# Optimization experiments

Measured on AMD Instinct MI355X. Metric: run time of the kernel, lower is better.

Reference implementation:

```python
import jax, jax.numpy as jnp
import numpy as np

B, N, K, H = 4, 2048, 30, 8
NUM_HIDDEN, NUM_IN, NUM_LATENT = 512, 640, 128
D = NUM_HIDDEN // H


def setup_inputs() -> dict:
    key = jax.random.key(0)
    ks = jax.random.split(key, 10)
    s = 0.05
    return {
        "z": jax.random.normal(ks[0], (B, NUM_LATENT), jnp.float32),
        "h_V": jax.random.normal(ks[1], (B, N, NUM_HIDDEN), jnp.float32),
        "h_E": jax.random.normal(ks[2], (B, N, K, NUM_IN), jnp.float32),
        "mask_attend": jnp.ones((B, N, K), jnp.float32),
        # weights stored as (in, out); torch Linear computes x @ W.T
        "W_Q": jax.random.normal(ks[3], (NUM_HIDDEN, NUM_HIDDEN), jnp.float32) * s,
        "W_K": jax.random.normal(ks[4], (NUM_IN, NUM_HIDDEN), jnp.float32) * s,
        "W_V": jax.random.normal(ks[5], (NUM_IN, NUM_HIDDEN), jnp.float32) * s,
        "W_O": jax.random.normal(ks[6], (NUM_HIDDEN, NUM_HIDDEN), jnp.float32) * s,
        "W_z": jax.random.normal(ks[7], (NUM_LATENT, K * H), jnp.float32) * s,
        "W_b": jax.random.normal(ks[8], (NUM_IN - 33, H), jnp.float32) * s,
    }


def reference(z, h_V, h_E, mask_attend, W_Q, W_K, W_V, W_O, W_z, W_b):
    b, n, k, _ = h_E.shape
    # projections
    Q = (h_V @ W_Q).reshape(b, n, H, D)            # [B,N,H,D]
    Kp = (h_E @ W_K).reshape(b, n, k, H, D)        # [B,N,K,H,D]
    V = (h_E @ W_V).reshape(b, n, k, H, D)         # [B,N,K,H,D]
    # per-neighbor dot-product scores -> [B,N,H,K]
    logits = jnp.einsum("bnhd,bnkhd->bnhk", Q, Kp) / np.sqrt(D).astype(np.float32)
    # latent bias: W_z output reshaped as (K, H) then transposed -> [B,1,H,K]
    bias_latent = (z @ W_z).reshape(b, 1, k, H).transpose(0, 1, 3, 2)
    # edge bias from h_E features past index 33 -> [B,N,H,K]
    bias_edges = (h_E[..., 33:] @ W_b).reshape(b, n, k, H).transpose(0, 1, 3, 2)
    logits = logits + bias_latent + bias_edges
    # masked, numerically stable softmax over K neighbors
    mask = mask_attend[:, :, None, :]              # [B,N,1,K] broadcast over heads
    neg_inf = jnp.finfo(jnp.float32).min
    logits = jnp.where(mask > 0, logits, neg_inf)
    attend = jax.nn.softmax(logits, axis=-1) * mask  # [B,N,H,K]
    # weighted aggregation of V, merge heads, output projection
    h_upd = jnp.einsum("bnhk,bnkhd->bnhd", attend, V).reshape(b, n, NUM_HIDDEN)
    return h_upd @ W_O
```

## Files before the change

kernel.cpp:

```cpp
#include <hip/hip_runtime.h>

#define B_      4
#define N_      2048
#define KN      30
#define H_      8
#define D_      64
#define CH      512
#define CI      640
#define CL      128
#define BN_TOT  8192

typedef unsigned short u16;
typedef unsigned int   u32;

typedef __attribute__((ext_vector_type(8))) short bf16x8;
typedef __attribute__((ext_vector_type(4))) float f32x4;

__device__ __forceinline__ float bf2f(u16 u) {
    return __uint_as_float(((u32)u) << 16);
}
__device__ __forceinline__ u16 f2bf(float f) {
    u32 u = __float_as_uint(f);
    return (u16)((u + 0x7FFFu + ((u >> 16) & 1u)) >> 16);
}

#define NEG_INF (-3.4028234663852886e38f)

__device__ __forceinline__ void async16(const void* g, void* l) {
    __builtin_amdgcn_global_load_lds(
        (const __attribute__((address_space(1))) unsigned int*)g,
        (__attribute__((address_space(3))) unsigned int*)l, 16, 0, 0);
}

__global__ __launch_bounds__(256) void cvt_kernel(
    const float* __restrict__ in, u16* __restrict__ out, int n)
{
    int i4 = (blockIdx.x * 256 + threadIdx.x) * 4;
    if (i4 < n) {
        float4 v = *(const float4*)&in[i4];
        ushort4 s;
        s.x = f2bf(v.x); s.y = f2bf(v.y); s.z = f2bf(v.z); s.w = f2bf(v.w);
        *(ushort4*)&out[i4] = s;
    }
}

__global__ __launch_bounds__(256) void cvt_t_kernel(
    const float* __restrict__ in, u16* __restrict__ out, int R, int Cc)
{
    int o = blockIdx.x * 256 + threadIdx.x;
    if (o < R * Cc) {
        int j = o / R, i = o - j * R;
        out[o] = f2bf(in[(size_t)i * Cc + j]);
    }
}

template<int BN, bool BF16OUT>
__global__ __launch_bounds__(256) void mfma_gemm(
    const u16* __restrict__ A, const u16* __restrict__ Bt, void* __restrict__ Cp,
    int K, int lda, int ldb, int ldc,
    long aHead, long bHead, long cHead, float alpha)
{
    constexpr int WN = BN / 2;
    constexpr int NT = WN / 16;
    constexpr int BR = (BN * 4) / 256;

    __shared__ u16 lA[128 * 32];
    __shared__ u16 lB[BN * 32];

    const int t    = threadIdx.x;
    const int w    = t >> 6;
    const int lane = t & 63;
    const int fr   = lane & 15;
    const int fq   = lane >> 4;
    const int wm   = w >> 1, wn = w & 1;
    const int m0   = blockIdx.y * 128;
    const int n0   = blockIdx.x * BN;

    const u16* Ah = A  + (size_t)blockIdx.z * aHead;
    const u16* Bh = Bt + (size_t)blockIdx.z * bHead;

    f32x4 zero = {0.f, 0.f, 0.f, 0.f};
    f32x4 acc[4][NT];
#pragma unroll
    for (int i = 0; i < 4; i++)
#pragma unroll
        for (int j = 0; j < NT; j++) acc[i][j] = zero;

    for (int k0 = 0; k0 < K; k0 += 32) {
#pragma unroll
        for (int r = 0; r < 2; r++) {
            int chunk = r * 256 + t;
            async16(Ah + (size_t)(m0 + (chunk >> 2)) * lda + k0 + ((chunk & 3) << 3),
                    &lA[(r * 256 + w * 64) * 8]);
        }
#pragma unroll
        for (int r = 0; r < BR; r++) {
            int chunk = r * 256 + t;
            async16(Bh + (size_t)(n0 + (chunk >> 2)) * ldb + k0 + ((chunk & 3) << 3),
                    &lB[(r * 256 + w * 64) * 8]);
        }
        __syncthreads();

        bf16x8 af[4], bfr[NT];
#pragma unroll
        for (int i = 0; i < 4; i++)
            af[i] = *(const bf16x8*)&lA[(wm * 64 + i * 16 + fr) * 32 + fq * 8];
#pragma unroll
        for (int j = 0; j < NT; j++)
            bfr[j] = *(const bf16x8*)&lB[(wn * WN + j * 16 + fr) * 32 + fq * 8];
#pragma unroll
        for (int i = 0; i < 4; i++)
#pragma unroll
            for (int j = 0; j < NT; j++)
                acc[i][j] = __builtin_amdgcn_mfma_f32_16x16x32_bf16(
                    af[i], bfr[j], acc[i][j], 0, 0, 0);
        __syncthreads();
    }

    const size_t cbase = (size_t)blockIdx.z * cHead;
#pragma unroll
    for (int i = 0; i < 4; i++) {
        int row = m0 + wm * 64 + i * 16 + fq * 4;
#pragma unroll
        for (int j = 0; j < NT; j++) {
            int col = n0 + wn * WN + j * 16 + fr;
#pragma unroll
            for (int r = 0; r < 4; r++) {
                float v = acc[i][j][r] * alpha;
                if (BF16OUT)
                    ((u16*)Cp)[cbase + (size_t)(row + r) * ldc + col] = f2bf(v);
                else
                    ((float*)Cp)[cbase + (size_t)(row + r) * ldc + col] = v;
            }
        }
    }
}

__global__ __launch_bounds__(256) void biasl_kernel(
    const float* __restrict__ z, const float* __restrict__ Wz,
    float* __restrict__ biasL)
{
    const int t = threadIdx.x;
    if (t < KN * H_) {
        for (int b = 0; b < B_; b++) {
            float s = 0.f;
            for (int l = 0; l < CL; l++) s += z[b * CL + l] * Wz[l * (KN * H_) + t];
            biasL[b * (KN * H_) + t] = s;
        }
    }
}

#define LDE 644

__global__ __launch_bounds__(256) void attn_kernel(
    const float* __restrict__ hE, const float* __restrict__ mask,
    const u16* Qt, const float* __restrict__ Wb,
    const float* __restrict__ biasL, u16* Eagg)
{
    __shared__ u16   ehs[KN * LDE];
    __shared__ float logit_s[H_ * KN];
    __shared__ float att_s[KN * H_];
    __shared__ float mask_s[KN];

    const int bn = blockIdx.x;
    const int b  = bn >> 11;
    const int t  = threadIdx.x;

    const float* he = hE + (size_t)bn * KN * CI;
    for (int idx = t; idx < KN * CI / 4; idx += 256) {
        int k = idx / 160;
        int c = (idx - k * 160) << 2;
        float4 v = *(const float4*)&he[k * CI + c];
        ushort4 sv;
        sv.x = f2bf(v.x); sv.y = f2bf(v.y); sv.z = f2bf(v.z); sv.w = f2bf(v.w);
        *(ushort4*)&ehs[k * LDE + c] = sv;
    }
    if (t < KN) mask_s[t] = mask[(size_t)bn * KN + t];
    __syncthreads();

    if (t < H_ * KN) {
        int h = t / KN, k = t - (t / KN) * KN;
        const u16* qrow = Qt + ((size_t)bn * H_ + h) * CI;
        const u16* erow = &ehs[k * LDE];
        float acc = 0.f;
        for (int c = 0; c < CI; c += 4) {
            ushort4 ev = *(const ushort4*)&erow[c];
            ushort4 qv = *(const ushort4*)&qrow[c];
            acc += bf2f(ev.x) * bf2f(qv.x) + bf2f(ev.y) * bf2f(qv.y)
                 + bf2f(ev.z) * bf2f(qv.z) + bf2f(ev.w) * bf2f(qv.w);
        }
        float acc2 = bf2f(erow[33]) * Wb[0 * H_ + h]
                   + bf2f(erow[34]) * Wb[1 * H_ + h]
                   + bf2f(erow[35]) * Wb[2 * H_ + h];
        for (int c = 36; c < CI; c += 4) {
            ushort4 ev = *(const ushort4*)&erow[c];
            const float* wb = &Wb[(c - 33) * H_ + h];
            acc2 += bf2f(ev.x) * wb[0] + bf2f(ev.y) * wb[8]
                  + bf2f(ev.z) * wb[16] + bf2f(ev.w) * wb[24];
        }
        float lg = acc + acc2 + biasL[b * (KN * H_) + k * H_ + h];
        lg = (mask_s[k] > 0.f) ? lg : NEG_INF;
        logit_s[h * KN + k] = lg;
    }
    __syncthreads();

    if (t < H_) {
        const int h = t;
        float m = NEG_INF;
#pragma unroll
        for (int k = 0; k < KN; k++) m = fmaxf(m, logit_s[h * KN + k]);
        float e[KN];
        float s = 0.f;
#pragma unroll
        for (int k = 0; k < KN; k++) { e[k] = __expf(logit_s[h * KN + k] - m); s += e[k]; }
        float inv = 1.f / s;
#pragma unroll
        for (int k = 0; k < KN; k++) att_s[k * H_ + h] = e[k] * inv * mask_s[k];
    }
    __syncthreads();

    if (t < 160) {
        const int c0 = t << 2;
        float acc[8][4] = {};
        for (int k = 0; k < KN; k++) {
            ushort4 ev = *(const ushort4*)&ehs[k * LDE + c0];
            float f0 = bf2f(ev.x), f1 = bf2f(ev.y), f2 = bf2f(ev.z), f3 = bf2f(ev.w);
            float4 a0 = *(const float4*)&att_s[k * H_];
            float4 a1 = *(const float4*)&att_s[k * H_ + 4];
            float aw[8] = {a0.x, a0.y, a0.z, a0.w, a1.x, a1.y, a1.z, a1.w};
#pragma unroll
            for (int h = 0; h < 8; h++) {
                acc[h][0] += aw[h] * f0; acc[h][1] += aw[h] * f1;
                acc[h][2] += aw[h] * f2; acc[h][3] += aw[h] * f3;
            }
        }
#pragma unroll
        for (int h = 0; h < 8; h++) {
            ushort4 sv;
            sv.x = f2bf(acc[h][0]); sv.y = f2bf(acc[h][1]);
            sv.z = f2bf(acc[h][2]); sv.w = f2bf(acc[h][3]);
            *(ushort4*)&Eagg[((size_t)bn * H_ + h) * CI + c0] = sv;
        }
    }
}

extern "C" void kernel_launch(void* const* d_in, const int* in_sizes, int n_in,
                              void* d_out, int out_size, void* d_ws, size_t ws_size,
                              hipStream_t stream)
{
    const float* z    = (const float*)d_in[0];
    const float* hV   = (const float*)d_in[1];
    const float* hE   = (const float*)d_in[2];
    const float* mask = (const float*)d_in[3];
    const float* WQ   = (const float*)d_in[4];
    const float* WK   = (const float*)d_in[5];
    const float* WV   = (const float*)d_in[6];
    const float* WO   = (const float*)d_in[7];
    const float* Wz   = (const float*)d_in[8];
    const float* Wb   = (const float*)d_in[9];
    float* out = (float*)d_out;

    char* w = (char*)d_ws;
    u16*   hV_bf = (u16*)w;
    u16*   Q_bf  = (u16*)(w + 8388608);
    u16*   Qt    = (u16*)(w + 16777216);
    u16*   WQt   = (u16*)(w + 100663296);
    u16*   WK_bf = (u16*)(w + 101187584);
    u16*   WVt   = (u16*)(w + 101842944);
    u16*   WOt   = (u16*)(w + 102498304);
    float* biasL = (float*)(w + 103022592);
    u16*   Eagg  = Qt;
    u16*   Hupd  = hV_bf;

    cvt_kernel<<<4096, 256, 0, stream>>>(hV, hV_bf, BN_TOT * CH);
    cvt_kernel<<<320, 256, 0, stream>>>(WK, WK_bf, CI * CH);
    cvt_t_kernel<<<1024, 256, 0, stream>>>(WQ, WQt, CH, CH);
    cvt_t_kernel<<<1280, 256, 0, stream>>>(WV, WVt, CI, CH);
    cvt_t_kernel<<<1024, 256, 0, stream>>>(WO, WOt, CH, CH);
    biasl_kernel<<<1, 256, 0, stream>>>(z, Wz, biasL);

    mfma_gemm<128, true><<<dim3(4, 64, 1), 256, 0, stream>>>(
        hV_bf, WQt, Q_bf, CH, CH, CH, CH, 0, 0, 0, 1.0f);
    mfma_gemm<128, true><<<dim3(5, 64, H_), 256, 0, stream>>>(
        Q_bf, WK_bf, Qt, 64, CH, CH, H_ * CI, 64, 64, CI, 0.125f);
    attn_kernel<<<dim3(BN_TOT), 256, 0, stream>>>(hE, mask, Qt, Wb, biasL, Eagg);
    mfma_gemm<64, true><<<dim3(1, 64, H_), 256, 0, stream>>>(
        Eagg, WVt, Hupd, CI, H_ * CI, CI, CH, CI, 64L * CI, 64, 1.0f);
    mfma_gemm<128, false><<<dim3(4, 64, 1), 256, 0, stream>>>(
        Hupd, WOt, out, CH, CH, CH, CH, 0, 0, 0, 1.0f);
}
```

Baseline: 1.291 ms.

## Fold edge bias into Q-tilde GEMM and compute attention logits with MFMA

Adds the W_b edge-bias weights to the per-head projected query vector in the Q·W_K^T GEMM epilogue, so the separate bias dot product over h_E columns disappears from the attention kernel. The logit computation (8 heads × 30 neighbors × 640 channels) now runs as 16x16x32 bf16 MFMAs on two waves instead of scalar FMA loops over 240 threads. The shared-memory h_E tile switches to an XOR-swizzled unpadded layout so the MFMA operand loads avoid bank conflicts. One risk is that the added bias is rounded to bf16 along with Qt, which slightly changes precision. Also, the MFMA rows beyond neighbor 29 are clamped and their duplicate results discarded.

```diff
diff --git a/kernel.cpp b/kernel.cpp
--- a/kernel.cpp
+++ b/kernel.cpp
@@ -54,11 +54,12 @@
     }
 }
 
-template<int BN, bool BF16OUT>
+template<int BN, bool BF16OUT, bool WBIAS>
 __global__ __launch_bounds__(256) void mfma_gemm(
     const u16* __restrict__ A, const u16* __restrict__ Bt, void* __restrict__ Cp,
     int K, int lda, int ldb, int ldc,
-    long aHead, long bHead, long cHead, float alpha)
+    long aHead, long bHead, long cHead, float alpha,
+    const float* __restrict__ wb)
 {
     constexpr int WN = BN / 2;
     constexpr int NT = WN / 16;
@@ -127,6 +128,9 @@
 #pragma unroll
             for (int r = 0; r < 4; r++) {
                 float v = acc[i][j][r] * alpha;
+                if (WBIAS) {
+                    if (col >= 33) v += wb[(size_t)(col - 33) * H_ + blockIdx.z];
+                }
                 if (BF16OUT)
                     ((u16*)Cp)[cbase + (size_t)(row + r) * ldc + col] = f2bf(v);
                 else
@@ -150,21 +154,25 @@
     }
 }
 
-#define LDE 644
+#define LGS 33
 
 __global__ __launch_bounds__(256) void attn_kernel(
     const float* __restrict__ hE, const float* __restrict__ mask,
-    const u16* Qt, const float* __restrict__ Wb,
-    const float* __restrict__ biasL, u16* Eagg)
-{
-    __shared__ u16   ehs[KN * LDE];
-    __shared__ float logit_s[H_ * KN];
+    const u16* Qt, const float* __restrict__ biasL, u16* Eagg)
+{
+    __shared__ __align__(16) u16 ehs[KN * CI];
+    __shared__ float logit_s[H_ * LGS];
     __shared__ float att_s[KN * H_];
     __shared__ float mask_s[KN];
 
-    const int bn = blockIdx.x;
-    const int b  = bn >> 11;
-    const int t  = threadIdx.x;
+    const int bn   = blockIdx.x;
+    const int b    = bn >> 11;
+    const int t    = threadIdx.x;
+    const int w    = t >> 6;
+    const int lane = t & 63;
+    const int fr   = lane & 15;
+    const int fq   = lane >> 4;
+    char* ebase = (char*)ehs;
 
     const float* he = hE + (size_t)bn * KN * CI;
     for (int idx = t; idx < KN * CI / 4; idx += 256) {
@@ -173,34 +181,35 @@
         float4 v = *(const float4*)&he[k * CI + c];
         ushort4 sv;
         sv.x = f2bf(v.x); sv.y = f2bf(v.y); sv.z = f2bf(v.z); sv.w = f2bf(v.w);
-        *(ushort4*)&ehs[k * LDE + c] = sv;
+        *(ushort4*)(ebase + ((k * 1280 + (c << 1)) ^ ((k & 7) << 4))) = sv;
     }
     if (t < KN) mask_s[t] = mask[(size_t)bn * KN + t];
     __syncthreads();
 
-    if (t < H_ * KN) {
-        int h = t / KN, k = t - (t / KN) * KN;
-        const u16* qrow = Qt + ((size_t)bn * H_ + h) * CI;
-        const u16* erow = &ehs[k * LDE];
-        float acc = 0.f;
-        for (int c = 0; c < CI; c += 4) {
-            ushort4 ev = *(const ushort4*)&erow[c];
-            ushort4 qv = *(const ushort4*)&qrow[c];
-            acc += bf2f(ev.x) * bf2f(qv.x) + bf2f(ev.y) * bf2f(qv.y)
-                 + bf2f(ev.z) * bf2f(qv.z) + bf2f(ev.w) * bf2f(qv.w);
-        }
-        float acc2 = bf2f(erow[33]) * Wb[0 * H_ + h]
-                   + bf2f(erow[34]) * Wb[1 * H_ + h]
-                   + bf2f(erow[35]) * Wb[2 * H_ + h];
-        for (int c = 36; c < CI; c += 4) {
-            ushort4 ev = *(const ushort4*)&erow[c];
-            const float* wb = &Wb[(c - 33) * H_ + h];
-            acc2 += bf2f(ev.x) * wb[0] + bf2f(ev.y) * wb[8]
-                  + bf2f(ev.z) * wb[16] + bf2f(ev.w) * wb[24];
-        }
-        float lg = acc + acc2 + biasL[b * (KN * H_) + k * H_ + h];
-        lg = (mask_s[k] > 0.f) ? lg : NEG_INF;
-        logit_s[h * KN + k] = lg;
+    if (w < 2) {
+        const u16* qrow = Qt + (size_t)bn * (H_ * CI) + (fr & 7) * CI + fq * 8;
+        int nr = w * 16 + fr;
+        if (nr > KN - 1) nr = KN - 1;
+        const char* erow = ebase + nr * 1280;
+        const int swz = (nr & 7) << 4;
+        f32x4 lacc = {0.f, 0.f, 0.f, 0.f};
+#pragma unroll 4
+        for (int kk = 0; kk < CI / 32; kk++) {
+            bf16x8 a  = *(const bf16x8*)(qrow + kk * 32);
+            bf16x8 bf = *(const bf16x8*)(erow + ((kk * 64 + fq * 16) ^ swz));
+            lacc = __builtin_amdgcn_mfma_f32_16x16x32_bf16(a, bf, lacc, 0, 0, 0);
+        }
+        int k = w * 16 + fr;
+        if (fq < 2 && k < KN) {
+            float mk = mask_s[k];
+            const float* blp = &biasL[b * (KN * H_) + k * H_];
+#pragma unroll
+            for (int r = 0; r < 4; r++) {
+                int h = fq * 4 + r;
+                float lg = lacc[r] + blp[h];
+                logit_s[h * LGS + k] = (mk > 0.f) ? lg : NEG_INF;
+            }
+        }
     }
     __syncthreads();
 
@@ -208,11 +217,11 @@
         const int h = t;
         float m = NEG_INF;
 #pragma unroll
-        for (int k = 0; k < KN; k++) m = fmaxf(m, logit_s[h * KN + k]);
+        for (int k = 0; k < KN; k++) m = fmaxf(m, logit_s[h * LGS + k]);
         float e[KN];
         float s = 0.f;
 #pragma unroll
-        for (int k = 0; k < KN; k++) { e[k] = __expf(logit_s[h * KN + k] - m); s += e[k]; }
+        for (int k = 0; k < KN; k++) { e[k] = __expf(logit_s[h * LGS + k] - m); s += e[k]; }
         float inv = 1.f / s;
 #pragma unroll
         for (int k = 0; k < KN; k++) att_s[k * H_ + h] = e[k] * inv * mask_s[k];
@@ -223,7 +232,7 @@
         const int c0 = t << 2;
         float acc[8][4] = {};
         for (int k = 0; k < KN; k++) {
-            ushort4 ev = *(const ushort4*)&ehs[k * LDE + c0];
+            ushort4 ev = *(const ushort4*)(ebase + ((k * 1280 + (c0 << 1)) ^ ((k & 7) << 4)));
             float f0 = bf2f(ev.x), f1 = bf2f(ev.y), f2 = bf2f(ev.z), f3 = bf2f(ev.w);
             float4 a0 = *(const float4*)&att_s[k * H_];
             float4 a1 = *(const float4*)&att_s[k * H_ + 4];
@@ -279,13 +288,13 @@
     cvt_t_kernel<<<1024, 256, 0, stream>>>(WO, WOt, CH, CH);
     biasl_kernel<<<1, 256, 0, stream>>>(z, Wz, biasL);
 
-    mfma_gemm<128, true><<<dim3(4, 64, 1), 256, 0, stream>>>(
-        hV_bf, WQt, Q_bf, CH, CH, CH, CH, 0, 0, 0, 1.0f);
-    mfma_gemm<128, true><<<dim3(5, 64, H_), 256, 0, stream>>>(
-        Q_bf, WK_bf, Qt, 64, CH, CH, H_ * CI, 64, 64, CI, 0.125f);
-    attn_kernel<<<dim3(BN_TOT), 256, 0, stream>>>(hE, mask, Qt, Wb, biasL, Eagg);
-    mfma_gemm<64, true><<<dim3(1, 64, H_), 256, 0, stream>>>(
-        Eagg, WVt, Hupd, CI, H_ * CI, CI, CH, CI, 64L * CI, 64, 1.0f);
-    mfma_gemm<128, false><<<dim3(4, 64, 1), 256, 0, stream>>>(
-        Hupd, WOt, out, CH, CH, CH, CH, 0, 0, 0, 1.0f);
-}
+    mfma_gemm<128, true, false><<<dim3(4, 64, 1), 256, 0, stream>>>(
+        hV_bf, WQt, Q_bf, CH, CH, CH, CH, 0, 0, 0, 1.0f, nullptr);
+    mfma_gemm<128, true, true><<<dim3(5, 64, H_), 256, 0, stream>>>(
+        Q_bf, WK_bf, Qt, 64, CH, CH, H_ * CI, 64, 64, CI, 0.125f, Wb);
+    attn_kernel<<<dim3(BN_TOT), 256, 0, stream>>>(hE, mask, Qt, biasL, Eagg);
+    mfma_gemm<64, true, false><<<dim3(1, 64, H_), 256, 0, stream>>>(
+        Eagg, WVt, Hupd, CI, H_ * CI, CI, CH, CI, 64L * CI, 64, 1.0f, nullptr);
+    mfma_gemm<128, false, false><<<dim3(4, 64, 1), 256, 0, stream>>>(
+        Hupd, WOt, out, CH, CH, CH, CH, 0, 0, 0, 1.0f, nullptr);
+}
```

New measurement: 1.082 ms. -16.2%, faster.
